# Kernel tuning notes

Hardware: AMD Instinct MI355X
Metric: run time of the kernel (lower is better)

The kernel has to match this reference:

```python
import jax, jax.numpy as jnp
import numpy as np

ALPHA = 1.702
LIMIT = 7.0
TOP_K = 4


def setup_inputs() -> dict:
    key = jax.random.key(0)
    ks = jax.random.split(key, 7)
    B, S, H, E, I = 2, 1024, 1024, 16, 2048
    scale_w = 1.0 / np.sqrt(H)
    return {
        "hidden_states": jax.random.normal(ks[0], (B, S, H), jnp.float32),
        "router_weight": jax.random.normal(ks[1], (E, H), jnp.float32) * scale_w,
        "router_bias": jax.random.normal(ks[2], (E,), jnp.float32) * 0.01,
        "gate_up_proj": jax.random.normal(ks[3], (E, H, 2 * I), jnp.float32) * scale_w,
        "gate_up_proj_bias": jax.random.normal(ks[4], (E, 2 * I), jnp.float32) * 0.01,
        "down_proj": jax.random.normal(ks[5], (E, I, H), jnp.float32) * (1.0 / np.sqrt(I)),
        "down_proj_bias": jax.random.normal(ks[6], (E, H), jnp.float32) * 0.01,
    }


def reference(hidden_states, router_weight, router_bias, gate_up_proj,
              gate_up_proj_bias, down_proj, down_proj_bias):
    B, S, H = hidden_states.shape
    E = router_weight.shape[0]
    dt = hidden_states.dtype

    # Router: linear -> softmax -> top-k -> renormalize
    router_logits = jnp.einsum('bsh,eh->bse', hidden_states, router_weight) + router_bias
    router_probs = jax.nn.softmax(router_logits, axis=-1)
    topk_weights, topk_indices = jax.lax.top_k(router_probs, TOP_K)  # [B,S,K]
    topk_weights = topk_weights / jnp.sum(topk_weights, axis=-1, keepdims=True)

    # Sparsity mask [B,S,E]: 1 for active experts (semantics of tt.sparse_matmul)
    onehot = jax.nn.one_hot(topk_indices, E, dtype=dt)        # [B,S,K,E]
    sparsity = jnp.sum(onehot, axis=2)                         # [B,S,E] (0/1)

    # Fused gate+up projection (interleaved layout), masked per-expert
    gate_up = jnp.einsum('bsh,ehf->bsef', hidden_states, gate_up_proj)  # [B,S,E,2I]
    gate_up = gate_up * sparsity[..., None]
    gate = gate_up[..., 0::2] + gate_up_proj_bias[:, 0::2]     # [B,S,E,I]
    up = gate_up[..., 1::2] + gate_up_proj_bias[:, 1::2]

    gate = jnp.minimum(gate, LIMIT)
    up = jnp.clip(up, -LIMIT, LIMIT)
    glu = gate * jax.nn.sigmoid(gate * ALPHA)
    activated = (up + 1.0) * glu                               # [B,S,E,I]

    # Down projection, masked per-expert, then bias
    down = jnp.einsum('bsei,eih->bseh', activated, down_proj)  # [B,S,E,H]
    down = down * sparsity[..., None] + down_proj_bias         # bias broadcasts [E,H]

    # Scatter top-k weights to full expert dim and combine
    full_weights = jnp.sum(onehot * topk_weights[..., None], axis=2)   # [B,S,E]
    output = jnp.sum(down * full_weights[..., None], axis=2)           # [B,S,H]
    return output, topk_weights
```

## Files before the change

kernel.cpp:

```cpp
#include <hip/hip_runtime.h>

#define TOKENS 2048
#define HD 1024
#define NEXP 16
#define TWO_I 4096
#define ID 2048

typedef short short8 __attribute__((ext_vector_type(8)));
typedef float f32x4 __attribute__((ext_vector_type(4)));
typedef unsigned short ushort;

static __device__ __forceinline__ ushort f2bf(float f) {
    union { float f; unsigned u; } v; v.f = f;
    unsigned r = v.u + 0x7FFFu + ((v.u >> 16) & 1u);
    return (ushort)(r >> 16);
}

static __device__ __forceinline__ void gload_lds16(const void* g, void* l) {
    __builtin_amdgcn_global_load_lds(
        (const __attribute__((address_space(1))) unsigned int*)(g),
        (__attribute__((address_space(3))) unsigned int*)(l), 16, 0, 0);
}

__global__ __launch_bounds__(256) void cvt_kernel(const float* __restrict__ hs,
                                                  ushort* __restrict__ hb) {
    int i = (blockIdx.x * 256 + threadIdx.x) * 4;
    float4 v = *(const float4*)(hs + i);
    union { ushort b[4]; float2 f2; } u;
    u.b[0] = f2bf(v.x); u.b[1] = f2bf(v.y); u.b[2] = f2bf(v.z); u.b[3] = f2bf(v.w);
    *(float2*)(hb + i) = u.f2;
}

__global__ __launch_bounds__(256) void transpose_cvt_kernel(
    const float* __restrict__ src, ushort* __restrict__ dst, int K, int N) {
    const int e = blockIdx.z;
    const int n0 = blockIdx.x * 64;
    const int k0 = blockIdx.y * 64;
    __shared__ float T[64][68];
    const float* s = src + (size_t)e * K * N + (size_t)k0 * N + n0;
    const int r = threadIdx.x >> 4;
    const int c4 = (threadIdx.x & 15) * 4;
#pragma unroll
    for (int i = 0; i < 64; i += 16) {
        float4 v = *(const float4*)(s + (size_t)(r + i) * N + c4);
        T[r + i][c4 + 0] = v.x; T[r + i][c4 + 1] = v.y;
        T[r + i][c4 + 2] = v.z; T[r + i][c4 + 3] = v.w;
    }
    __syncthreads();
    const int n = threadIdx.x >> 2;
    const int kc = (threadIdx.x & 3) * 16;
    union { ushort b[16]; short8 v[2]; } o;
#pragma unroll
    for (int j = 0; j < 16; ++j) o.b[j] = f2bf(T[kc + j][n]);
    ushort* d = dst + (size_t)e * N * K + (size_t)(n0 + n) * K + k0 + kc;
    *(short8*)(d) = o.v[0];
    *(short8*)(d + 8) = o.v[1];
}

__global__ __launch_bounds__(256) void router_kernel(
    const float* __restrict__ hs, const float* __restrict__ rw,
    const float* __restrict__ rb, float* __restrict__ topk_w_out,
    int* __restrict__ topk_idx, int* __restrict__ counts) {
    const int wave = threadIdx.x >> 6;
    const int lane = threadIdx.x & 63;
    const int t = blockIdx.x * 4 + wave;

    float h[16];
#pragma unroll
    for (int j = 0; j < 16; ++j) h[j] = hs[t * HD + j * 64 + lane];

    __shared__ float lg[4][NEXP];
#pragma unroll
    for (int e = 0; e < NEXP; ++e) {
        float acc = 0.f;
#pragma unroll
        for (int j = 0; j < 16; ++j) acc += h[j] * rw[e * HD + j * 64 + lane];
#pragma unroll
        for (int s = 32; s > 0; s >>= 1) acc += __shfl_xor(acc, s);
        if (lane == 0) lg[wave][e] = acc + rb[e];
    }
    if (lane == 0) {
        float mx = lg[wave][0];
        for (int e = 1; e < NEXP; ++e) mx = fmaxf(mx, lg[wave][e]);
        float pr[NEXP];
        for (int e = 0; e < NEXP; ++e) pr[e] = __expf(lg[wave][e] - mx);
        int idx[4]; float wv[4]; float sum4 = 0.f;
        for (int k = 0; k < 4; ++k) {
            int bi = 0; float bv = -1.f;
            for (int e = 0; e < NEXP; ++e)
                if (pr[e] > bv) { bv = pr[e]; bi = e; }
            idx[k] = bi; wv[k] = bv; pr[bi] = -2.f; sum4 += bv;
        }
        for (int k = 0; k < 4; ++k) {
            topk_w_out[t * 4 + k] = wv[k] / sum4;
            topk_idx[t * 4 + k] = idx[k];
            atomicAdd(&counts[idx[k]], 1);
        }
    }
}

__global__ void scan_kernel(const int* __restrict__ counts, int* __restrict__ offsets,
                            int* __restrict__ cursor) {
    if (threadIdx.x == 0 && blockIdx.x == 0) {
        int o = 0;
        for (int e = 0; e < NEXP; ++e) { offsets[e] = o; cursor[e] = o; o += counts[e]; }
        offsets[NEXP] = o;
    }
}

__global__ __launch_bounds__(256) void build_kernel(
    const int* __restrict__ topk_idx, const float* __restrict__ topk_w,
    int* __restrict__ cursor, int* __restrict__ token_list, float* __restrict__ slot_w,
    int* __restrict__ slot_of) {
    int t = blockIdx.x * 256 + threadIdx.x;
    for (int k = 0; k < 4; ++k) {
        int e = topk_idx[t * 4 + k];
        int pos = atomicAdd(&cursor[e], 1);
        token_list[pos] = t;
        slot_w[pos] = topk_w[t * 4 + k];
        slot_of[t * 4 + k] = pos;
    }
}


__global__ __launch_bounds__(256) void gemm1_t_kernel(
    const ushort* __restrict__ hb, const ushort* __restrict__ gupT,
    const float* __restrict__ gub, const int* __restrict__ offsets,
    const int* __restrict__ token_list, ushort* __restrict__ act) {
    const int e = blockIdx.z;
    const int so = offsets[e];
    const int ne = offsets[e + 1] - so;
    const int row0 = blockIdx.y * 128;
    if (row0 >= ne) return;
    const int n0 = blockIdx.x * 128;

    __shared__ ushort As[2][4096];
    __shared__ ushort Bs[2][4096];

    const int tid = threadIdx.x;
    const int lane = tid & 63;
    const int w = tid >> 6;
    const int m = lane & 15;
    const int q = lane >> 4;
    const int wm = (w >> 1) * 64;
    const int wn = (w & 1) * 64;
    const int qa = (q ^ (m & 3)) * 8;

    const int r0 = tid >> 2;
    const int ce = (((tid & 3) ^ (r0 & 3)) * 8);
    int ar0 = row0 + r0;       if (ar0 >= ne) ar0 = ne - 1;
    int ar1 = row0 + 64 + r0;  if (ar1 >= ne) ar1 = ne - 1;
    const ushort* ga0 = hb + (size_t)token_list[so + ar0] * HD + ce;
    const ushort* ga1 = hb + (size_t)token_list[so + ar1] * HD + ce;
    const ushort* gb0 = gupT + (size_t)e * TWO_I * HD + (size_t)(n0 + r0) * HD + ce;
    const ushort* gb1 = gb0 + (size_t)64 * HD;

    f32x4 acc[4][4] = {};

#define STAGE1(B, K0) do { \
    gload_lds16(ga0 + (K0), As[B] + w * 512); \
    gload_lds16(ga1 + (K0), As[B] + 2048 + w * 512); \
    gload_lds16(gb0 + (K0), Bs[B] + w * 512); \
    gload_lds16(gb1 + (K0), Bs[B] + 2048 + w * 512); \
} while (0)

#define COMPUTE1(B) do { \
    short8 af[4], bfr[4]; \
    _Pragma("unroll") for (int rt = 0; rt < 4; ++rt) \
        af[rt] = *(const short8*)(As[B] + (wm + rt * 16 + m) * 32 + qa); \
    _Pragma("unroll") for (int c = 0; c < 4; ++c) \
        bfr[c] = *(const short8*)(Bs[B] + (wn + c * 16 + m) * 32 + qa); \
    _Pragma("unroll") for (int rt = 0; rt < 4; ++rt) \
        _Pragma("unroll") for (int c = 0; c < 4; ++c) \
            acc[rt][c] = __builtin_amdgcn_mfma_f32_16x16x32_bf16(af[rt], bfr[c], acc[rt][c], 0, 0, 0); \
} while (0)

    STAGE1(0, 0);
    int cur = 0;
    for (int t = 0; t < HD / 32 - 1; ++t) {
        STAGE1(cur ^ 1, (t + 1) * 32);
        asm volatile("s_waitcnt vmcnt(4)" ::: "memory");
        __builtin_amdgcn_s_barrier();
        __builtin_amdgcn_s_setprio(1);
        COMPUTE1(cur);
        __builtin_amdgcn_s_setprio(0);
        __builtin_amdgcn_s_barrier();
        cur ^= 1;
    }
    asm volatile("s_waitcnt vmcnt(0)" ::: "memory");
    __builtin_amdgcn_s_barrier();
    COMPUTE1(cur);

#pragma unroll
    for (int c = 0; c < 4; ++c) {
        const int n = n0 + wn + c * 16 + m;
        const float bias = gub[e * TWO_I + n];
#pragma unroll
        for (int rt = 0; rt < 4; ++rt) {
#pragma unroll
            for (int rr = 0; rr < 4; ++rr) {
                const int grow = row0 + wm + rt * 16 + q * 4 + rr;
                float v = acc[rt][c][rr] + bias;
                float pv = __shfl_xor(v, 1);
                float gate = (m & 1) ? pv : v;
                float up   = (m & 1) ? v : pv;
                gate = fminf(gate, 7.0f);
                up = fminf(fmaxf(up, -7.0f), 7.0f);
                float glu = gate / (1.0f + __expf(-1.702f * gate));
                float a = (up + 1.0f) * glu;
                if (!(m & 1) && grow < ne)
                    act[(size_t)(so + grow) * ID + (n >> 1)] = f2bf(a);
            }
        }
    }
}

__global__ __launch_bounds__(256) void gemm2_t_kernel(
    const ushort* __restrict__ act, const ushort* __restrict__ downT,
    const int* __restrict__ offsets, float* __restrict__ dslot) {
    const int e = blockIdx.z;
    const int so = offsets[e];
    const int ne = offsets[e + 1] - so;
    const int row0 = blockIdx.y * 128;
    if (row0 >= ne) return;
    const int n0 = blockIdx.x * 128;

    __shared__ ushort As[2][4096];
    __shared__ ushort Bs[2][4096];

    const int tid = threadIdx.x;
    const int lane = tid & 63;
    const int w = tid >> 6;
    const int m = lane & 15;
    const int q = lane >> 4;
    const int wm = (w >> 1) * 64;
    const int wn = (w & 1) * 64;
    const int qa = (q ^ (m & 3)) * 8;

    const int r0 = tid >> 2;
    const int ce = (((tid & 3) ^ (r0 & 3)) * 8);
    const ushort* ga0 = act + (size_t)(so + row0 + r0) * ID + ce;
    const ushort* ga1 = ga0 + (size_t)64 * ID;
    const ushort* gb0 = downT + (size_t)e * HD * ID + (size_t)(n0 + r0) * ID + ce;
    const ushort* gb1 = gb0 + (size_t)64 * ID;

    f32x4 acc[4][4] = {};

#define STAGE2(B, K0) do { \
    gload_lds16(ga0 + (K0), As[B] + w * 512); \
    gload_lds16(ga1 + (K0), As[B] + 2048 + w * 512); \
    gload_lds16(gb0 + (K0), Bs[B] + w * 512); \
    gload_lds16(gb1 + (K0), Bs[B] + 2048 + w * 512); \
} while (0)

#define COMPUTE2(B) do { \
    short8 af[4], bfr[4]; \
    _Pragma("unroll") for (int rt = 0; rt < 4; ++rt) \
        af[rt] = *(const short8*)(As[B] + (wm + rt * 16 + m) * 32 + qa); \
    _Pragma("unroll") for (int c = 0; c < 4; ++c) \
        bfr[c] = *(const short8*)(Bs[B] + (wn + c * 16 + m) * 32 + qa); \
    _Pragma("unroll") for (int rt = 0; rt < 4; ++rt) \
        _Pragma("unroll") for (int c = 0; c < 4; ++c) \
            acc[rt][c] = __builtin_amdgcn_mfma_f32_16x16x32_bf16(af[rt], bfr[c], acc[rt][c], 0, 0, 0); \
} while (0)

    STAGE2(0, 0);
    int cur = 0;
    for (int t = 0; t < ID / 32 - 1; ++t) {
        STAGE2(cur ^ 1, (t + 1) * 32);
        asm volatile("s_waitcnt vmcnt(4)" ::: "memory");
        __builtin_amdgcn_s_barrier();
        __builtin_amdgcn_s_setprio(1);
        COMPUTE2(cur);
        __builtin_amdgcn_s_setprio(0);
        __builtin_amdgcn_s_barrier();
        cur ^= 1;
    }
    asm volatile("s_waitcnt vmcnt(0)" ::: "memory");
    __builtin_amdgcn_s_barrier();
    COMPUTE2(cur);

#pragma unroll
    for (int rt = 0; rt < 4; ++rt) {
#pragma unroll
        for (int rr = 0; rr < 4; ++rr) {
            const int grow = row0 + wm + rt * 16 + q * 4 + rr;
            if (grow < ne) {
                float* dp = dslot + (size_t)(so + grow) * HD + n0 + wn + m;
#pragma unroll
                for (int c = 0; c < 4; ++c) dp[c * 16] = acc[rt][c][rr];
            }
        }
    }
}

__global__ __launch_bounds__(256) void combine_kernel(
    const float* __restrict__ dslot, const float* __restrict__ dwb,
    const int* __restrict__ topk_idx, const int* __restrict__ slot_of,
    const float* __restrict__ topk_w, float* __restrict__ out) {
    const int t = blockIdx.x;
    const int n = threadIdx.x * 4;
    float4 o = {0.f, 0.f, 0.f, 0.f};
#pragma unroll
    for (int k = 0; k < 4; ++k) {
        const int e = topk_idx[t * 4 + k];
        const int s = slot_of[t * 4 + k];
        const float wgt = topk_w[t * 4 + k];
        float4 d = *(const float4*)(dslot + (size_t)s * HD + n);
        float4 b = *(const float4*)(dwb + (size_t)e * HD + n);
        o.x += wgt * (d.x + b.x);
        o.y += wgt * (d.y + b.y);
        o.z += wgt * (d.z + b.z);
        o.w += wgt * (d.w + b.w);
    }
    *(float4*)(out + (size_t)t * HD + n) = o;
}


__global__ __launch_bounds__(256) void gemm1_fb_kernel(
    const ushort* __restrict__ hb, const float* __restrict__ gup,
    const float* __restrict__ gub, const int* __restrict__ offsets,
    const int* __restrict__ token_list, ushort* __restrict__ act) {
    const int e = blockIdx.z;
    const int so = offsets[e];
    const int ne = offsets[e + 1] - so;
    const int row0 = blockIdx.y * 64;
    if (row0 >= ne) return;
    const int n0 = blockIdx.x * 64;
    __shared__ ushort Al[64][40];
    __shared__ ushort Bt[64][40];
    const int tid = threadIdx.x;
    const int lane = tid & 63;
    const int wave = tid >> 6;
    const int m = lane & 15;
    const int q = lane >> 4;
    const int ar = tid >> 2;
    const int ac = (tid & 3) * 8;
    int arow = row0 + ar; if (arow >= ne) arow = ne - 1;
    const int tok = token_list[so + arow];
    const ushort* aptr = hb + tok * HD + ac;
    const int bk = tid >> 3;
    const int bn = (tid & 7) * 8;
    const float* bptr = gup + (size_t)e * HD * TWO_I + (size_t)bk * TWO_I + n0 + bn;
    f32x4 acc[4] = {{0,0,0,0},{0,0,0,0},{0,0,0,0},{0,0,0,0}};
    for (int k0 = 0; k0 < HD; k0 += 32) {
        float4 av = *(const float4*)(aptr + k0);
        *(float4*)(&Al[ar][ac]) = av;
        const float* bp = bptr + (size_t)k0 * TWO_I;
        float4 b0 = *(const float4*)(bp);
        float4 b1 = *(const float4*)(bp + 4);
        Bt[bn + 0][bk] = f2bf(b0.x); Bt[bn + 1][bk] = f2bf(b0.y);
        Bt[bn + 2][bk] = f2bf(b0.z); Bt[bn + 3][bk] = f2bf(b0.w);
        Bt[bn + 4][bk] = f2bf(b1.x); Bt[bn + 5][bk] = f2bf(b1.y);
        Bt[bn + 6][bk] = f2bf(b1.z); Bt[bn + 7][bk] = f2bf(b1.w);
        __syncthreads();
        short8 af = *(const short8*)(&Al[wave * 16 + m][q * 8]);
#pragma unroll
        for (int c = 0; c < 4; ++c) {
            short8 bf = *(const short8*)(&Bt[c * 16 + m][q * 8]);
            acc[c] = __builtin_amdgcn_mfma_f32_16x16x32_bf16(af, bf, acc[c], 0, 0, 0);
        }
        __syncthreads();
    }
#pragma unroll
    for (int c = 0; c < 4; ++c) {
        const int n = n0 + c * 16 + m;
        const float bias = gub[e * TWO_I + n];
#pragma unroll
        for (int r = 0; r < 4; ++r) {
            const int grow = row0 + wave * 16 + q * 4 + r;
            float v = acc[c][r] + bias;
            float pv = __shfl_xor(v, 1);
            float gate = (m & 1) ? pv : v;
            float up   = (m & 1) ? v : pv;
            gate = fminf(gate, 7.0f);
            up = fminf(fmaxf(up, -7.0f), 7.0f);
            float glu = gate / (1.0f + __expf(-1.702f * gate));
            float a = (up + 1.0f) * glu;
            if (!(m & 1) && grow < ne)
                act[(size_t)(so + grow) * ID + (n >> 1)] = f2bf(a);
        }
    }
}

__global__ __launch_bounds__(256) void gemm2_fb_kernel(
    const ushort* __restrict__ act, const float* __restrict__ dwp,
    const float* __restrict__ dwb, const int* __restrict__ offsets,
    const int* __restrict__ token_list, const float* __restrict__ slot_w,
    float* __restrict__ out) {
    const int e = blockIdx.z;
    const int so = offsets[e];
    const int ne = offsets[e + 1] - so;
    const int row0 = blockIdx.y * 64;
    if (row0 >= ne) return;
    const int n0 = blockIdx.x * 64;
    __shared__ ushort Al[64][40];
    __shared__ ushort Bt[64][40];
    const int tid = threadIdx.x;
    const int lane = tid & 63;
    const int wave = tid >> 6;
    const int m = lane & 15;
    const int q = lane >> 4;
    const int ar = tid >> 2;
    const int ac = (tid & 3) * 8;
    int arow = row0 + ar; if (arow >= ne) arow = ne - 1;
    const ushort* aptr = act + (size_t)(so + arow) * ID + ac;
    const int bk = tid >> 3;
    const int bn = (tid & 7) * 8;
    const float* bptr = dwp + (size_t)e * ID * HD + (size_t)bk * HD + n0 + bn;
    f32x4 acc[4] = {{0,0,0,0},{0,0,0,0},{0,0,0,0},{0,0,0,0}};
    for (int k0 = 0; k0 < ID; k0 += 32) {
        float4 av = *(const float4*)(aptr + k0);
        *(float4*)(&Al[ar][ac]) = av;
        const float* bp = bptr + (size_t)k0 * HD;
        float4 b0 = *(const float4*)(bp);
        float4 b1 = *(const float4*)(bp + 4);
        Bt[bn + 0][bk] = f2bf(b0.x); Bt[bn + 1][bk] = f2bf(b0.y);
        Bt[bn + 2][bk] = f2bf(b0.z); Bt[bn + 3][bk] = f2bf(b0.w);
        Bt[bn + 4][bk] = f2bf(b1.x); Bt[bn + 5][bk] = f2bf(b1.y);
        Bt[bn + 6][bk] = f2bf(b1.z); Bt[bn + 7][bk] = f2bf(b1.w);
        __syncthreads();
        short8 af = *(const short8*)(&Al[wave * 16 + m][q * 8]);
#pragma unroll
        for (int c = 0; c < 4; ++c) {
            short8 bf = *(const short8*)(&Bt[c * 16 + m][q * 8]);
            acc[c] = __builtin_amdgcn_mfma_f32_16x16x32_bf16(af, bf, acc[c], 0, 0, 0);
        }
        __syncthreads();
    }
#pragma unroll
    for (int r = 0; r < 4; ++r) {
        const int grow = row0 + wave * 16 + q * 4 + r;
        if (grow < ne) {
            const int slot = so + grow;
            const int tok = token_list[slot];
            const float wgt = slot_w[slot];
#pragma unroll
            for (int c = 0; c < 4; ++c) {
                const int n = n0 + c * 16 + m;
                atomicAdd(&out[tok * HD + n], (acc[c][r] + dwb[e * HD + n]) * wgt);
            }
        }
    }
}

extern "C" void kernel_launch(void* const* d_in, const int* in_sizes, int n_in,
                              void* d_out, int out_size, void* d_ws, size_t ws_size,
                              hipStream_t stream) {
    const float* hs  = (const float*)d_in[0];
    const float* rw  = (const float*)d_in[1];
    const float* rb  = (const float*)d_in[2];
    const float* gup = (const float*)d_in[3];
    const float* gub = (const float*)d_in[4];
    const float* dwp = (const float*)d_in[5];
    const float* dwb = (const float*)d_in[6];

    float* out = (float*)d_out;
    float* topk_w = out + (size_t)TOKENS * HD;

    char* w = (char*)d_ws;
    int* counts     = (int*)(w + 0);
    int* cursor     = (int*)(w + 64);
    int* offsets    = (int*)(w + 128);
    int* token_list = (int*)(w + 256);
    float* slot_w   = (float*)(w + 256 + 32768);
    int* topk_idx   = (int*)(w + 256 + 65536);
    int* slot_of    = (int*)(w + 256 + 98304);
    ushort* hb      = (ushort*)(w + ((size_t)1 << 20));
    ushort* act     = (ushort*)(w + ((size_t)6 << 20));
    ushort* gupT    = (ushort*)(w + ((size_t)41 << 20));
    ushort* downT   = (ushort*)(w + ((size_t)169 << 20));
    float* dslot    = (float*)(w + ((size_t)233 << 20));
    const size_t need = (size_t)266 << 20;

    hipMemsetAsync(w, 0, 256, stream);

    cvt_kernel<<<2048, 256, 0, stream>>>(hs, hb);
    router_kernel<<<512, 256, 0, stream>>>(hs, rw, rb, topk_w, topk_idx, counts);
    scan_kernel<<<1, 64, 0, stream>>>(counts, offsets, cursor);
    build_kernel<<<8, 256, 0, stream>>>(topk_idx, topk_w, cursor, token_list, slot_w, slot_of);

    if (ws_size >= need) {
        transpose_cvt_kernel<<<dim3(TWO_I / 64, HD / 64, NEXP), 256, 0, stream>>>(
            gup, gupT, HD, TWO_I);
        transpose_cvt_kernel<<<dim3(HD / 64, ID / 64, NEXP), 256, 0, stream>>>(
            dwp, downT, ID, HD);
        gemm1_t_kernel<<<dim3(TWO_I / 128, TOKENS / 128, NEXP), 256, 0, stream>>>(
            hb, gupT, gub, offsets, token_list, act);
        gemm2_t_kernel<<<dim3(HD / 128, TOKENS / 128, NEXP), 256, 0, stream>>>(
            act, downT, offsets, dslot);
        combine_kernel<<<TOKENS, 256, 0, stream>>>(dslot, dwb, topk_idx, slot_of, topk_w, out);
    } else {
        hipMemsetAsync(out, 0, (size_t)TOKENS * HD * sizeof(float), stream);
        gemm1_fb_kernel<<<dim3(TWO_I / 64, TOKENS / 64, NEXP), 256, 0, stream>>>(
            hb, gup, gub, offsets, token_list, act);
        gemm2_fb_kernel<<<dim3(HD / 64, TOKENS / 64, NEXP), 256, 0, stream>>>(
            act, dwp, dwb, offsets, token_list, slot_w, out);
    }
}
```

Measured before the change: 848.1 us.

## Triple-buffer GEMM loads, drop LDS swizzle, and fuse small preprocessing kernels

The GEMM main loops move from double to triple buffering, so global-to-LDS loads run two stages ahead and wait with a deeper vmcnt. The XOR swizzle on LDS tile addresses is removed in both GEMMs. The bf16 activation conversion is folded into the router kernel, scan and build become a single one-block kernel with atomics in shared memory, and the two weight transpose launches are merged into one grid. These cut launch count and global-memory latency stalls, but removing the swizzle may bring back LDS bank conflicts, and the extra LDS buffer may lower occupancy.

Measured after the change: 805.2 us. -5.1%, faster.

```diff
diff --git a/kernel.cpp b/kernel.cpp
--- a/kernel.cpp
+++ b/kernel.cpp
@@ -22,45 +22,23 @@
         (__attribute__((address_space(3))) unsigned int*)(l), 16, 0, 0);
 }
 
-__global__ __launch_bounds__(256) void cvt_kernel(const float* __restrict__ hs,
-                                                  ushort* __restrict__ hb) {
-    int i = (blockIdx.x * 256 + threadIdx.x) * 4;
-    float4 v = *(const float4*)(hs + i);
-    union { ushort b[4]; float2 f2; } u;
-    u.b[0] = f2bf(v.x); u.b[1] = f2bf(v.y); u.b[2] = f2bf(v.z); u.b[3] = f2bf(v.w);
-    *(float2*)(hb + i) = u.f2;
-}
-
-__global__ __launch_bounds__(256) void transpose_cvt_kernel(
-    const float* __restrict__ src, ushort* __restrict__ dst, int K, int N) {
-    const int e = blockIdx.z;
-    const int n0 = blockIdx.x * 64;
-    const int k0 = blockIdx.y * 64;
-    __shared__ float T[64][68];
-    const float* s = src + (size_t)e * K * N + (size_t)k0 * N + n0;
-    const int r = threadIdx.x >> 4;
-    const int c4 = (threadIdx.x & 15) * 4;
-#pragma unroll
-    for (int i = 0; i < 64; i += 16) {
-        float4 v = *(const float4*)(s + (size_t)(r + i) * N + c4);
-        T[r + i][c4 + 0] = v.x; T[r + i][c4 + 1] = v.y;
-        T[r + i][c4 + 2] = v.z; T[r + i][c4 + 3] = v.w;
-    }
-    __syncthreads();
-    const int n = threadIdx.x >> 2;
-    const int kc = (threadIdx.x & 3) * 16;
-    union { ushort b[16]; short8 v[2]; } o;
-#pragma unroll
-    for (int j = 0; j < 16; ++j) o.b[j] = f2bf(T[kc + j][n]);
-    ushort* d = dst + (size_t)e * N * K + (size_t)(n0 + n) * K + k0 + kc;
-    *(short8*)(d) = o.v[0];
-    *(short8*)(d + 8) = o.v[1];
-}
-
 __global__ __launch_bounds__(256) void router_kernel(
     const float* __restrict__ hs, const float* __restrict__ rw,
     const float* __restrict__ rb, float* __restrict__ topk_w_out,
-    int* __restrict__ topk_idx, int* __restrict__ counts) {
+    int* __restrict__ topk_idx, int* __restrict__ counts,
+    ushort* __restrict__ hb) {
+    {
+        const int i = blockIdx.x * 4096 + threadIdx.x * 16;
+#pragma unroll
+        for (int j = 0; j < 4; ++j) {
+            float4 v = *(const float4*)(hs + i + j * 4);
+            union { ushort b[4]; float2 f2; } u;
+            u.b[0] = f2bf(v.x); u.b[1] = f2bf(v.y);
+            u.b[2] = f2bf(v.z); u.b[3] = f2bf(v.w);
+            *(float2*)(hb + i + j * 4) = u.f2;
+        }
+    }
+
     const int wave = threadIdx.x >> 6;
     const int lane = threadIdx.x & 63;
     const int t = blockIdx.x * 4 + wave;
@@ -99,27 +77,63 @@
     }
 }
 
-__global__ void scan_kernel(const int* __restrict__ counts, int* __restrict__ offsets,
-                            int* __restrict__ cursor) {
-    if (threadIdx.x == 0 && blockIdx.x == 0) {
+__global__ __launch_bounds__(256) void scanbuild_kernel(
+    const int* __restrict__ counts, int* __restrict__ offsets,
+    const int* __restrict__ topk_idx, const float* __restrict__ topk_w,
+    int* __restrict__ token_list, float* __restrict__ slot_w,
+    int* __restrict__ slot_of) {
+    __shared__ int cur_s[NEXP];
+    if (threadIdx.x == 0) {
         int o = 0;
-        for (int e = 0; e < NEXP; ++e) { offsets[e] = o; cursor[e] = o; o += counts[e]; }
+        for (int e = 0; e < NEXP; ++e) { offsets[e] = o; cur_s[e] = o; o += counts[e]; }
         offsets[NEXP] = o;
     }
-}
-
-__global__ __launch_bounds__(256) void build_kernel(
-    const int* __restrict__ topk_idx, const float* __restrict__ topk_w,
-    int* __restrict__ cursor, int* __restrict__ token_list, float* __restrict__ slot_w,
-    int* __restrict__ slot_of) {
-    int t = blockIdx.x * 256 + threadIdx.x;
-    for (int k = 0; k < 4; ++k) {
-        int e = topk_idx[t * 4 + k];
-        int pos = atomicAdd(&cursor[e], 1);
-        token_list[pos] = t;
-        slot_w[pos] = topk_w[t * 4 + k];
-        slot_of[t * 4 + k] = pos;
-    }
+    __syncthreads();
+    for (int t = threadIdx.x; t < TOKENS; t += 256) {
+#pragma unroll
+        for (int k = 0; k < 4; ++k) {
+            int e = topk_idx[t * 4 + k];
+            int pos = atomicAdd(&cur_s[e], 1);
+            token_list[pos] = t;
+            slot_w[pos] = topk_w[t * 4 + k];
+            slot_of[t * 4 + k] = pos;
+        }
+    }
+}
+
+__global__ __launch_bounds__(256) void transpose_cvt2_kernel(
+    const float* __restrict__ gup, ushort* __restrict__ gupT,
+    const float* __restrict__ dwp, ushort* __restrict__ downT) {
+    const int e = blockIdx.z;
+    const float* src; ushort* dst;
+    int K, N, n0, k0;
+    if (blockIdx.y < 16) {
+        src = gup; dst = gupT; K = HD; N = TWO_I;
+        n0 = blockIdx.x * 64; k0 = blockIdx.y * 64;
+    } else {
+        src = dwp; dst = downT; K = ID; N = HD;
+        const int idx = (blockIdx.y - 16) * 64 + blockIdx.x;
+        n0 = (idx & 15) * 64; k0 = (idx >> 4) * 64;
+    }
+    __shared__ float T[64][68];
+    const float* s = src + (size_t)e * K * N + (size_t)k0 * N + n0;
+    const int r = threadIdx.x >> 4;
+    const int c4 = (threadIdx.x & 15) * 4;
+#pragma unroll
+    for (int i = 0; i < 64; i += 16) {
+        float4 v = *(const float4*)(s + (size_t)(r + i) * N + c4);
+        T[r + i][c4 + 0] = v.x; T[r + i][c4 + 1] = v.y;
+        T[r + i][c4 + 2] = v.z; T[r + i][c4 + 3] = v.w;
+    }
+    __syncthreads();
+    const int n = threadIdx.x >> 2;
+    const int kc = (threadIdx.x & 3) * 16;
+    union { ushort b[16]; short8 v[2]; } o;
+#pragma unroll
+    for (int j = 0; j < 16; ++j) o.b[j] = f2bf(T[kc + j][n]);
+    ushort* d = dst + (size_t)e * N * K + (size_t)(n0 + n) * K + k0 + kc;
+    *(short8*)(d) = o.v[0];
+    *(short8*)(d + 8) = o.v[1];
 }
 
 
@@ -134,8 +148,8 @@
     if (row0 >= ne) return;
     const int n0 = blockIdx.x * 128;
 
-    __shared__ ushort As[2][4096];
-    __shared__ ushort Bs[2][4096];
+    __shared__ ushort As[3][4096];
+    __shared__ ushort Bs[3][4096];
 
     const int tid = threadIdx.x;
     const int lane = tid & 63;
@@ -144,10 +158,9 @@
     const int q = lane >> 4;
     const int wm = (w >> 1) * 64;
     const int wn = (w & 1) * 64;
-    const int qa = (q ^ (m & 3)) * 8;
 
     const int r0 = tid >> 2;
-    const int ce = (((tid & 3) ^ (r0 & 3)) * 8);
+    const int ce = (tid & 3) * 8;
     int ar0 = row0 + r0;       if (ar0 >= ne) ar0 = ne - 1;
     int ar1 = row0 + 64 + r0;  if (ar1 >= ne) ar1 = ne - 1;
     const ushort* ga0 = hb + (size_t)token_list[so + ar0] * HD + ce;
@@ -167,26 +180,32 @@
 #define COMPUTE1(B) do { \
     short8 af[4], bfr[4]; \
     _Pragma("unroll") for (int rt = 0; rt < 4; ++rt) \
-        af[rt] = *(const short8*)(As[B] + (wm + rt * 16 + m) * 32 + qa); \
+        af[rt] = *(const short8*)(As[B] + (wm + rt * 16 + m) * 32 + q * 8); \
     _Pragma("unroll") for (int c = 0; c < 4; ++c) \
-        bfr[c] = *(const short8*)(Bs[B] + (wn + c * 16 + m) * 32 + qa); \
+        bfr[c] = *(const short8*)(Bs[B] + (wn + c * 16 + m) * 32 + q * 8); \
     _Pragma("unroll") for (int rt = 0; rt < 4; ++rt) \
         _Pragma("unroll") for (int c = 0; c < 4; ++c) \
             acc[rt][c] = __builtin_amdgcn_mfma_f32_16x16x32_bf16(af[rt], bfr[c], acc[rt][c], 0, 0, 0); \
 } while (0)
 
     STAGE1(0, 0);
+    STAGE1(1, 32);
     int cur = 0;
-    for (int t = 0; t < HD / 32 - 1; ++t) {
-        STAGE1(cur ^ 1, (t + 1) * 32);
-        asm volatile("s_waitcnt vmcnt(4)" ::: "memory");
+    for (int t = 0; t < HD / 32 - 2; ++t) {
+        int nxt = cur + 2; if (nxt >= 3) nxt -= 3;
+        STAGE1(nxt, (t + 2) * 32);
+        asm volatile("s_waitcnt vmcnt(8)" ::: "memory");
         __builtin_amdgcn_s_barrier();
         __builtin_amdgcn_s_setprio(1);
         COMPUTE1(cur);
         __builtin_amdgcn_s_setprio(0);
         __builtin_amdgcn_s_barrier();
-        cur ^= 1;
-    }
+        cur = (cur == 2) ? 0 : cur + 1;
+    }
+    asm volatile("s_waitcnt vmcnt(4)" ::: "memory");
+    __builtin_amdgcn_s_barrier();
+    COMPUTE1(cur);
+    cur = (cur == 2) ? 0 : cur + 1;
     asm volatile("s_waitcnt vmcnt(0)" ::: "memory");
     __builtin_amdgcn_s_barrier();
     COMPUTE1(cur);
@@ -225,8 +244,8 @@
     if (row0 >= ne) return;
     const int n0 = blockIdx.x * 128;
 
-    __shared__ ushort As[2][4096];
-    __shared__ ushort Bs[2][4096];
+    __shared__ ushort As[3][4096];
+    __shared__ ushort Bs[3][4096];
 
     const int tid = threadIdx.x;
     const int lane = tid & 63;
@@ -235,10 +254,9 @@
     const int q = lane >> 4;
     const int wm = (w >> 1) * 64;
     const int wn = (w & 1) * 64;
-    const int qa = (q ^ (m & 3)) * 8;
 
     const int r0 = tid >> 2;
-    const int ce = (((tid & 3) ^ (r0 & 3)) * 8);
+    const int ce = (tid & 3) * 8;
     const ushort* ga0 = act + (size_t)(so + row0 + r0) * ID + ce;
     const ushort* ga1 = ga0 + (size_t)64 * ID;
     const ushort* gb0 = downT + (size_t)e * HD * ID + (size_t)(n0 + r0) * ID + ce;
@@ -256,26 +274,32 @@
 #define COMPUTE2(B) do { \
     short8 af[4], bfr[4]; \
     _Pragma("unroll") for (int rt = 0; rt < 4; ++rt) \
-        af[rt] = *(const short8*)(As[B] + (wm + rt * 16 + m) * 32 + qa); \
+        af[rt] = *(const short8*)(As[B] + (wm + rt * 16 + m) * 32 + q * 8); \
     _Pragma("unroll") for (int c = 0; c < 4; ++c) \
-        bfr[c] = *(const short8*)(Bs[B] + (wn + c * 16 + m) * 32 + qa); \
+        bfr[c] = *(const short8*)(Bs[B] + (wn + c * 16 + m) * 32 + q * 8); \
     _Pragma("unroll") for (int rt = 0; rt < 4; ++rt) \
         _Pragma("unroll") for (int c = 0; c < 4; ++c) \
             acc[rt][c] = __builtin_amdgcn_mfma_f32_16x16x32_bf16(af[rt], bfr[c], acc[rt][c], 0, 0, 0); \
 } while (0)
 
     STAGE2(0, 0);
+    STAGE2(1, 32);
     int cur = 0;
-    for (int t = 0; t < ID / 32 - 1; ++t) {
-        STAGE2(cur ^ 1, (t + 1) * 32);
-        asm volatile("s_waitcnt vmcnt(4)" ::: "memory");
+    for (int t = 0; t < ID / 32 - 2; ++t) {
+        int nxt = cur + 2; if (nxt >= 3) nxt -= 3;
+        STAGE2(nxt, (t + 2) * 32);
+        asm volatile("s_waitcnt vmcnt(8)" ::: "memory");
         __builtin_amdgcn_s_barrier();
         __builtin_amdgcn_s_setprio(1);
         COMPUTE2(cur);
         __builtin_amdgcn_s_setprio(0);
         __builtin_amdgcn_s_barrier();
-        cur ^= 1;
-    }
+        cur = (cur == 2) ? 0 : cur + 1;
+    }
+    asm volatile("s_waitcnt vmcnt(4)" ::: "memory");
+    __builtin_amdgcn_s_barrier();
+    COMPUTE2(cur);
+    cur = (cur == 2) ? 0 : cur + 1;
     asm volatile("s_waitcnt vmcnt(0)" ::: "memory");
     __builtin_amdgcn_s_barrier();
     COMPUTE2(cur);
@@ -460,7 +484,6 @@
 
     char* w = (char*)d_ws;
     int* counts     = (int*)(w + 0);
-    int* cursor     = (int*)(w + 64);
     int* offsets    = (int*)(w + 128);
     int* token_list = (int*)(w + 256);
     float* slot_w   = (float*)(w + 256 + 32768);
@@ -473,18 +496,15 @@
     float* dslot    = (float*)(w + ((size_t)233 << 20));
     const size_t need = (size_t)266 << 20;
 
-    hipMemsetAsync(w, 0, 256, stream);
-
-    cvt_kernel<<<2048, 256, 0, stream>>>(hs, hb);
-    router_kernel<<<512, 256, 0, stream>>>(hs, rw, rb, topk_w, topk_idx, counts);
-    scan_kernel<<<1, 64, 0, stream>>>(counts, offsets, cursor);
-    build_kernel<<<8, 256, 0, stream>>>(topk_idx, topk_w, cursor, token_list, slot_w, slot_of);
+    hipMemsetAsync(w, 0, 128, stream);
+
+    router_kernel<<<512, 256, 0, stream>>>(hs, rw, rb, topk_w, topk_idx, counts, hb);
+    scanbuild_kernel<<<1, 256, 0, stream>>>(counts, offsets, topk_idx, topk_w,
+                                            token_list, slot_w, slot_of);
 
     if (ws_size >= need) {
-        transpose_cvt_kernel<<<dim3(TWO_I / 64, HD / 64, NEXP), 256, 0, stream>>>(
-            gup, gupT, HD, TWO_I);
-        transpose_cvt_kernel<<<dim3(HD / 64, ID / 64, NEXP), 256, 0, stream>>>(
-            dwp, downT, ID, HD);
+        transpose_cvt2_kernel<<<dim3(64, 24, NEXP), 256, 0, stream>>>(
+            gup, gupT, dwp, downT);
         gemm1_t_kernel<<<dim3(TWO_I / 128, TOKENS / 128, NEXP), 256, 0, stream>>>(
             hb, gupT, gub, offsets, token_list, act);
         gemm2_t_kernel<<<dim3(HD / 128, TOKENS / 128, NEXP), 256, 0, stream>>>(
```
